# Optimization experiments

Hardware: AMD Instinct MI355X
Metric: run time of the kernel (lower is better)

Reference implementation:

```python
import jax, jax.numpy as jnp
import numpy as np
import math

KMAX = 4
K_FLOOR = 1e-6
NUM_GRAPHS = 32

def _k_lattice():
    r = np.arange(-KMAX, KMAX + 1)
    I, J, Kk = np.meshgrid(r, r, r, indexing='ij')
    lat = np.stack([I, J, Kk], axis=-1).reshape(-1, 3).astype(np.float32)
    lat = lat[np.any(lat != 0, axis=1)]  # exclude k=0 (include_k0=False)
    return jnp.asarray(lat)  # [K,3], K=728

def setup_inputs() -> dict:
    key = jax.random.key(0)
    ks = jax.random.split(key, 10)
    N, B, C, H = 8192, NUM_GRAPHS, 4, 64
    pos = jax.random.uniform(ks[0], (N, 3), dtype=jnp.float32) * 10.0
    batch = jnp.sort(jax.random.randint(ks[1], (N,), 0, B)).astype(jnp.int32)
    cell = jnp.eye(3, dtype=jnp.float32)[None] * 12.0 + 0.2 * jax.random.normal(ks[2], (B, 3, 3), dtype=jnp.float32)
    source = 0.1 * jax.random.normal(ks[3], (N, C), dtype=jnp.float32)
    W1 = jax.random.normal(ks[4], (3, H), dtype=jnp.float32) * (1.0 / math.sqrt(3))
    b1 = jnp.zeros((H,), jnp.float32)
    W2 = jax.random.normal(ks[5], (H, H), dtype=jnp.float32) * (1.0 / math.sqrt(H))
    b2 = jnp.zeros((H,), jnp.float32)
    W3 = jax.random.normal(ks[6], (H, 1), dtype=jnp.float32) * (1.0 / math.sqrt(H))
    b3 = jnp.zeros((1,), jnp.float32)
    return {"pos": pos, "batch": batch, "cell": cell, "source": source,
            "W1": W1, "b1": b1, "W2": W2, "b2": b2, "W3": W3, "b3": b3}

def reference(pos, batch, cell, source, W1, b1, W2, b2, W3, b3):
    two_pi = 2.0 * math.pi
    klat = _k_lattice()                              # [K,3]
    B = cell.shape[0]
    inv_cells = jnp.linalg.inv(cell)                 # [B,3,3]
    # fractional coords and phases
    frac = jnp.einsum('ni,nij->nj', pos, inv_cells[batch])   # [N,3]
    phases = two_pi * (frac @ klat.T)                # [N,K]
    cosP = jnp.cos(phases)
    sinP = jnp.sin(phases)
    # structure factors via segment-sum over graphs
    w_cos = source[:, None, :] * cosP[:, :, None]    # [N,K,C]
    w_sin = source[:, None, :] * sinP[:, :, None]
    S_cos = jax.ops.segment_sum(w_cos, batch, num_segments=B)  # [B,K,C]
    S_sin = jax.ops.segment_sum(w_sin, batch, num_segments=B)
    # k-space radial filter
    k_cart = two_pi * jnp.einsum('kd,bdh->bkh', klat, inv_cells)  # [B,K,3]
    k_norms = jnp.linalg.norm(k_cart, axis=-1)       # [B,K]
    safe_k = jnp.maximum(k_norms, K_FLOOR)
    x0 = jnp.log1p(safe_k)
    feat = jnp.stack([x0, x0 * x0, 1.0 / safe_k], axis=-1)       # [B,K,3]
    h = jax.nn.silu(feat @ W1 + b1)
    h = jax.nn.silu(h @ W2 + b2)
    scale = jax.nn.softplus((h @ W3 + b3)[..., 0])   # [B,K]
    w = (4.0 * math.pi / (safe_k * safe_k)) * scale
    w = jnp.where(k_norms > K_FLOOR, w, 0.0)         # include_k0=False
    volumes = jnp.maximum(jnp.abs(jnp.linalg.det(cell)), K_FLOOR)  # [B]
    # per-atom potential
    t_cos = w[batch] * cosP                          # [N,K]
    t_sin = w[batch] * sinP
    potential = (jnp.einsum('nk,nkc->nc', t_cos, S_cos[batch]) +
                 jnp.einsum('nk,nkc->nc', t_sin, S_sin[batch])) / volumes[batch][:, None]
    atom_energy = 0.5 * jnp.sum(source * potential, axis=-1, keepdims=True)  # [N,1]
    return atom_energy
```

## Files before the change

### kernel.cpp

```cpp
#include <hip/hip_runtime.h>
#include <math.h>

#define N_ATOMS 8192
#define NGRAPH  32
#define KHALF   364
#define TWO_PI  6.28318530717958647692f


__device__ __forceinline__ float silu_f(float x) {
    return x / (1.0f + __expf(-x));
}

__device__ __forceinline__ void screv(float rev, float* s, float* c) {
    float f = rev - floorf(rev);
    *s = __builtin_amdgcn_sinf(f);
    *c = __builtin_amdgcn_cosf(f);
}

__device__ __forceinline__ void inv3x3(const float* __restrict__ c, float* iv, float* detOut) {
    float a00 = c[0], a01 = c[1], a02 = c[2];
    float a10 = c[3], a11 = c[4], a12 = c[5];
    float a20 = c[6], a21 = c[7], a22 = c[8];
    float c00 = a11 * a22 - a12 * a21;
    float c01 = a12 * a20 - a10 * a22;
    float c02 = a10 * a21 - a11 * a20;
    float det = a00 * c00 + a01 * c01 + a02 * c02;
    float r = 1.0f / det;
    iv[0] = c00 * r; iv[1] = (a02 * a21 - a01 * a22) * r; iv[2] = (a01 * a12 - a02 * a11) * r;
    iv[3] = c01 * r; iv[4] = (a00 * a22 - a02 * a20) * r; iv[5] = (a02 * a10 - a00 * a12) * r;
    iv[6] = c02 * r; iv[7] = (a01 * a20 - a00 * a21) * r; iv[8] = (a00 * a11 - a01 * a10) * r;
    *detOut = det;
}

__device__ __forceinline__ int lower_bound_wave(const int* __restrict__ batch, int v, int lane) {
    int x = batch[lane * 128];
    int c1 = __popcll(__ballot(x < v));
    int lo2 = (c1 > 0 ? c1 - 1 : 0) * 128;
    int y = batch[lo2 + lane * 2];
    int c2 = __popcll(__ballot(y < v));
    if (c2 == 0) return lo2;
    int cand = lo2 + 2 * c2;
    return (batch[cand - 1] < v) ? cand : cand - 1;
}

__device__ __forceinline__ void tab_fill(float2* __restrict__ t9, float c1, float s1) {
    float c2 = c1 * c1 - s1 * s1, s2 = 2.f * c1 * s1;
    float c3 = c2 * c1 - s2 * s1, s3 = c2 * s1 + s2 * c1;
    float c4 = c2 * c2 - s2 * s2, s4 = 2.f * c2 * s2;
    t9[4] = make_float2(1.f, 0.f);
    t9[5] = make_float2(c1, s1);
    t9[3] = make_float2(c1, -s1);
    t9[6] = make_float2(c2, s2);
    t9[2] = make_float2(c2, -s2);
    t9[7] = make_float2(c3, s3);
    t9[1] = make_float2(c3, -s3);
    t9[8] = make_float2(c4, s4);
    t9[0] = make_float2(c4, -s4);
}

__global__ __launch_bounds__(512) void kAll(
    const float* __restrict__ cell, const float* __restrict__ pos,
    const int* __restrict__ batch, const float* __restrict__ source,
    const float* __restrict__ W1, const float* __restrict__ b1,
    const float* __restrict__ W2, const float* __restrict__ b2,
    const float* __restrict__ W3, const float* __restrict__ b3,
    float* __restrict__ out)
{
    __shared__ float2 tab[128][3][9];
    __shared__ float4 srcs[128];
    __shared__ float4 partC[7][64];
    __shared__ float4 partS[7][64];
    __shared__ float  comb[512];
    __shared__ int    sbounds[2];
    __shared__ float  lw[64];
    __shared__ float4 lSc[64];
    __shared__ float4 lSs[64];

    int bid = blockIdx.x;
    int tid = threadIdx.x;
    int gb = bid >> 3;
    int b  = bid & 7;

    int pA, jA0, jA1, jB0, jB1, nsegA, nel;
    if (b < 4) { pA = b;     jA0 = 0; jA1 = 5; jB0 = 0; jB1 = 0; nsegA = 45; nel = 45; }
    else       { pA = b - 4; jA0 = 5; jA1 = 9;
                 jB0 = b - 4; jB1 = (b == 7) ? 5 : (b - 3);
                 nsegA = 36; nel = 36 + (jB1 - jB0) * 9; }
    int nrows  = (jA1 - jA0) + (jB1 - jB0);
    int rsplit = (nrows + 1) >> 1;

    int kl = tid & 63;
    int h  = tid >> 6;

    if (h >= 6) {
        int lb = lower_bound_wave(batch, gb + (h - 6), kl);
        if (kl == 0) sbounds[h - 6] = lb;
    }

    float iv[9]; float det;
    inv3x3(cell + gb * 9, iv, &det);
    float vol = fmaxf(fabsf(det), 1e-6f);

    int el = kl;
    int pe, jje, lle;
    if (el < nsegA) { pe = pA; jje = jA0 + el / 9; lle = el % 9; }
    else            { int e2 = el - nsegA; pe = 4; jje = jB0 + e2 / 9; lle = e2 % 9; }
    int hk = pe * 81 + jje * 9 + lle;
    bool evalid = (el < nel) && (hk < KHALF);

    {
        float fi = (float)(pe - 4);
        float fj = (float)(jje - 4);
        float fl = (float)(lle - 4);
        float kx = TWO_PI * (fi * iv[0] + fj * iv[3] + fl * iv[6]);
        float ky = TWO_PI * (fi * iv[1] + fj * iv[4] + fl * iv[7]);
        float kz = TWO_PI * (fi * iv[2] + fj * iv[5] + fl * iv[8]);
        float kn = sqrtf(kx * kx + ky * ky + kz * kz);
        float sk = fmaxf(kn, 1e-6f);
        float x0 = log1pf(sk);
        float f0 = x0, f1 = x0 * x0, f2 = 1.0f / sk;

        float acc[8];
        #pragma unroll
        for (int j = 0; j < 8; ++j) acc[j] = b2[h * 8 + j];
        for (int i = 0; i < 64; ++i) {
            float a = b1[i] + f0 * W1[i] + f1 * W1[64 + i] + f2 * W1[128 + i];
            float hh = silu_f(a);
            const float* w2row = W2 + i * 64 + h * 8;
            #pragma unroll
            for (int j = 0; j < 8; ++j) acc[j] = fmaf(hh, w2row[j], acc[j]);
        }
        float partial = 0.f;
        #pragma unroll
        for (int j = 0; j < 8; ++j) partial += silu_f(acc[j]) * W3[h * 8 + j];
        comb[tid] = partial;
        __syncthreads();
        if (h == 0) {
            float mlp = b3[0];
            #pragma unroll
            for (int w = 0; w < 8; ++w) mlp += comb[kl + 64 * w];
            float sc = (mlp > 20.0f) ? mlp : log1pf(__expf(mlp));
            float wgt = (12.566370614359172954f / (sk * sk)) * sc;
            if (!(kn > 1e-6f)) wgt = 0.0f;
            lw[kl] = evalid ? (wgt / vol) : 0.0f;
        }
    }

    int s0 = sbounds[0], e0 = sbounds[1];

    float4 accC = make_float4(0.f, 0.f, 0.f, 0.f);
    float4 accS = make_float4(0.f, 0.f, 0.f, 0.f);

    for (int base = s0; base < e0; base += 128) {
        int cnt = min(128, e0 - base);
        __syncthreads();
        {
            int a    = tid & 127;
            int dsel = tid >> 7;
            if (a < cnt) {
                int n = base + a;
                if (dsel < 3) {
                    float px = pos[n * 3], py = pos[n * 3 + 1], pz = pos[n * 3 + 2];
                    float ph = px * iv[dsel] + py * iv[3 + dsel] + pz * iv[6 + dsel];
                    float s1, c1; screv(ph, &s1, &c1);
                    tab_fill(&tab[a][dsel][0], c1, s1);
                } else {
                    srcs[a] = ((const float4*)source)[n];
                }
            }
        }
        __syncthreads();

        if (evalid) {
            for (int a = h; a < cnt; a += 8) {
                float2 ti = tab[a][0][pe];
                float2 tj = tab[a][1][jje];
                float2 tl = tab[a][2][lle];
                float c12 = ti.x * tj.x - ti.y * tj.y;
                float s12 = ti.x * tj.y + ti.y * tj.x;
                float cv = c12 * tl.x - s12 * tl.y;
                float sv = c12 * tl.y + s12 * tl.x;
                float4 s = srcs[a];
                accC.x = fmaf(s.x, cv, accC.x); accC.y = fmaf(s.y, cv, accC.y);
                accC.z = fmaf(s.z, cv, accC.z); accC.w = fmaf(s.w, cv, accC.w);
                accS.x = fmaf(s.x, sv, accS.x); accS.y = fmaf(s.y, sv, accS.y);
                accS.z = fmaf(s.z, sv, accS.z); accS.w = fmaf(s.w, sv, accS.w);
            }
        }
    }

    if (h > 0) {
        partC[h - 1][kl] = accC;
        partS[h - 1][kl] = accS;
    }
    __syncthreads();
    if (h == 0) {
        #pragma unroll
        for (int qq = 0; qq < 7; ++qq) {
            float4 pc = partC[qq][kl], ps = partS[qq][kl];
            accC.x += pc.x; accC.y += pc.y; accC.z += pc.z; accC.w += pc.w;
            accS.x += ps.x; accS.y += ps.y; accS.z += ps.z; accS.w += ps.w;
        }
        lSc[kl] = accC;
        lSs[kl] = accS;
    }
    __syncthreads();

    int half = tid >> 8;
    int r0 = half ? rsplit : 0;
    int r1 = half ? nrows  : rsplit;
    int g = 4 - pA;

    for (int na = (tid & 255); s0 + na < e0; na += 256) {
        int n = s0 + na;
        float px = pos[n * 3], py = pos[n * 3 + 1], pz = pos[n * 3 + 2];
        float p1 = px * iv[0] + py * iv[3] + pz * iv[6];
        float p2 = px * iv[1] + py * iv[4] + pz * iv[7];
        float p3 = px * iv[2] + py * iv[5] + pz * iv[8];
        float s1, c1; screv(p1, &s1, &c1);
        float s2, c2; screv(p2, &s2, &c2);
        float s3, c3; screv(p3, &s3, &c3);
        float c3_2 = c3 * c3 - s3 * s3, s3_2 = 2.f * c3 * s3;
        float c3_4 = c3_2 * c3_2 - s3_2 * s3_2, s3_4 = 2.f * c3_2 * s3_2;
        float c2_2 = c2 * c2 - s2 * s2, s2_2 = 2.f * c2 * s2;
        float c2_4 = c2_2 * c2_2 - s2_2 * s2_2, s2_4 = 2.f * c2_2 * s2_2;
        float4 s = ((const float4*)source)[n];

        float acc = 0.f;
        int rr = 0;

        {
            float cg_, sg_;
            if (g == 1)      { cg_ = c1; sg_ = s1; }
            else {
                float c2p = c1 * c1 - s1 * s1, s2p = 2.f * c1 * s1;
                if (g == 2)      { cg_ = c2p; sg_ = s2p; }
                else if (g == 3) { cg_ = c2p * c1 - s2p * s1; sg_ = s2p * c1 + c2p * s1; }
                else             { cg_ = c2p * c2p - s2p * s2p; sg_ = 2.f * c2p * s2p; }
            }
            float ci0 = cg_, si0 = -sg_;

            float ejc, ejs;
            if (jA0 == 0) {
                ejc = ci0 * c2_4 + si0 * s2_4;
                ejs = si0 * c2_4 - ci0 * s2_4;
            } else {
                ejc = ci0 * c2 - si0 * s2;
                ejs = si0 * c2 + ci0 * s2;
            }

            for (int jj = jA0; jj < jA1; ++jj, ++rr) {
                if (rr >= r0 && rr < r1) {
                    float fc = ejc * c3_4 + ejs * s3_4;
                    float fs = ejs * c3_4 - ejc * s3_4;
                    #pragma unroll
                    for (int ll = 0; ll < 9; ++ll) {
                        int e = rr * 9 + ll;
                        float4 C  = lSc[e];
                        float4 S4 = lSs[e];
                        float w_ = lw[e];
                        float dc = s.x * C.x  + s.y * C.y  + s.z * C.z  + s.w * C.w;
                        float ds = s.x * S4.x + s.y * S4.y + s.z * S4.z + s.w * S4.w;
                        acc = fmaf(w_, fmaf(fc, dc, fs * ds), acc);
                        float nfc = fc * c3 - fs * s3;
                        fs = fc * s3 + fs * c3;
                        fc = nfc;
                    }
                }
                float nejc = ejc * c2 - ejs * s2;
                ejs = ejc * s2 + ejs * c2;
                ejc = nejc;
            }
        }

        if (jB1 > jB0) {
            float ejc = c2_4, ejs = -s2_4;
            for (int t = 0; t < jB0; ++t) {
                float nf = ejc * c2 - ejs * s2;
                ejs = ejc * s2 + ejs * c2;
                ejc = nf;
            }
            for (int jj = jB0; jj < jB1; ++jj, ++rr) {
                if (rr >= r0 && rr < r1) {
                    float fc = ejc * c3_4 + ejs * s3_4;
                    float fs = ejs * c3_4 - ejc * s3_4;
                    #pragma unroll
                    for (int ll = 0; ll < 9; ++ll) {
                        int e = rr * 9 + ll;
                        float4 C  = lSc[e];
                        float4 S4 = lSs[e];
                        float w_ = lw[e];
                        float dc = s.x * C.x  + s.y * C.y  + s.z * C.z  + s.w * C.w;
                        float ds = s.x * S4.x + s.y * S4.y + s.z * S4.z + s.w * S4.w;
                        acc = fmaf(w_, fmaf(fc, dc, fs * ds), acc);
                        float nfc = fc * c3 - fs * s3;
                        fs = fc * s3 + fs * c3;
                        fc = nfc;
                    }
                }
                float nejc = ejc * c2 - ejs * s2;
                ejs = ejc * s2 + ejs * c2;
                ejc = nejc;
            }
        }

        atomicAdd(&out[n], acc);
    }
}

extern "C" void kernel_launch(void* const* d_in, const int* in_sizes, int n_in,
                              void* d_out, int out_size, void* d_ws, size_t ws_size,
                              hipStream_t stream)
{
    const float* pos    = (const float*)d_in[0];
    const int*   batch  = (const int*)d_in[1];
    const float* cell   = (const float*)d_in[2];
    const float* source = (const float*)d_in[3];
    const float* W1 = (const float*)d_in[4];
    const float* b1 = (const float*)d_in[5];
    const float* W2 = (const float*)d_in[6];
    const float* b2 = (const float*)d_in[7];
    const float* W3 = (const float*)d_in[8];
    const float* b3 = (const float*)d_in[9];
    float* out = (float*)d_out;
    (void)d_ws; (void)ws_size;

    kAll<<<dim3(NGRAPH * 8), 512, 0, stream>>>(cell, pos, batch, source,
        W1, b1, W2, b2, W3, b3, out);
}
```

Before: 92.97 us.

## Stage per-atom phase tables once and reuse them in potential phase

Enlarges the atom chunk to 384 so a typical graph of about 256 atoms fits in one pass. Each atom's phase table is built once per block, holding only the rows this block needs, and is reused by both the structure-factor and potential phases instead of recomputing sin/cos per atom. MLP weights are copied into shared memory, global atom loads are issued before the MLP so their latency overlaps it, and the softplus reduction moves to wave 1. This adds a large shared-memory footprint with launch_bounds(512,1), keeps a fallback path for graphs over 384 atoms, and removes the block barrier inside the MLP.

```diff
diff --git a/kernel.cpp b/kernel.cpp
--- a/kernel.cpp
+++ b/kernel.cpp
@@ -5,6 +5,7 @@
 #define NGRAPH  32
 #define KHALF   364
 #define TWO_PI  6.28318530717958647692f
+#define CH      384
 
 
 __device__ __forceinline__ float silu_f(float x) {
@@ -43,22 +44,58 @@
     return (batch[cand - 1] < v) ? cand : cand - 1;
 }
 
-__device__ __forceinline__ void tab_fill(float2* __restrict__ t9, float c1, float s1) {
-    float c2 = c1 * c1 - s1 * s1, s2 = 2.f * c1 * s1;
-    float c3 = c2 * c1 - s2 * s1, s3 = c2 * s1 + s2 * c1;
-    float c4 = c2 * c2 - s2 * s2, s4 = 2.f * c2 * s2;
-    t9[4] = make_float2(1.f, 0.f);
-    t9[5] = make_float2(c1, s1);
-    t9[3] = make_float2(c1, -s1);
-    t9[6] = make_float2(c2, s2);
-    t9[2] = make_float2(c2, -s2);
-    t9[7] = make_float2(c3, s3);
-    t9[1] = make_float2(c3, -s3);
-    t9[8] = make_float2(c4, s4);
-    t9[0] = make_float2(c4, -s4);
-}
-
-__global__ __launch_bounds__(512) void kAll(
+__device__ __forceinline__ void stage_atom(
+    float2 (* __restrict__ atab)[17], float4* __restrict__ srcs, int a,
+    float px, float py, float pz, float4 msrc, const float* __restrict__ iv,
+    int g, int jA0, int jA1, int jB0, int jB1)
+{
+    float r1 = px * iv[0] + py * iv[3] + pz * iv[6];
+    float r2 = px * iv[1] + py * iv[4] + pz * iv[7];
+    float r3 = px * iv[2] + py * iv[5] + pz * iv[8];
+    float s1, c1; screv(r1, &s1, &c1);
+    float s2, c2; screv(r2, &s2, &c2);
+    float s3, c3; screv(r3, &s3, &c3);
+    float c1_2 = c1 * c1 - s1 * s1, s1_2 = 2.f * c1 * s1;
+    float cg_, sg_;
+    if (g == 1)      { cg_ = c1;   sg_ = s1; }
+    else if (g == 2) { cg_ = c1_2; sg_ = s1_2; }
+    else if (g == 3) { cg_ = c1_2 * c1 - s1_2 * s1; sg_ = s1_2 * c1 + c1_2 * s1; }
+    else             { cg_ = c1_2 * c1_2 - s1_2 * s1_2; sg_ = 2.f * c1_2 * s1_2; }
+    atab[a][0] = make_float2(cg_, -sg_);
+    float c2_2 = c2 * c2 - s2 * s2, s2_2 = 2.f * c2 * s2;
+    float c2_4 = c2_2 * c2_2 - s2_2 * s2_2, s2_4 = 2.f * c2_2 * s2_2;
+    float ec, es;
+    if (jA0 == 0) { ec = c2_4; es = -s2_4; } else { ec = c2; es = s2; }
+    int slot = 1;
+    for (int m = jA0; m < jA1; ++m) {
+        atab[a][slot] = make_float2(ec, es); ++slot;
+        float t = ec * c2 - es * s2; es = ec * s2 + es * c2; ec = t;
+    }
+    if (jB1 > jB0) {
+        int q = 4 - jB0;
+        float qc, qs;
+        if (q == 4)      { qc = c2_4; qs = s2_4; }
+        else if (q == 3) { qc = c2_2 * c2 - s2_2 * s2; qs = s2_2 * c2 + c2_2 * s2; }
+        else if (q == 2) { qc = c2_2; qs = s2_2; }
+        else             { qc = c2;   qs = s2; }
+        ec = qc; es = -qs;
+        for (int m = jB0; m < jB1; ++m) {
+            atab[a][slot] = make_float2(ec, es); ++slot;
+            float t = ec * c2 - es * s2; es = ec * s2 + es * c2; ec = t;
+        }
+    }
+    float c3_2 = c3 * c3 - s3 * s3, s3_2 = 2.f * c3 * s3;
+    float c3_4 = c3_2 * c3_2 - s3_2 * s3_2, s3_4 = 2.f * c3_2 * s3_2;
+    ec = c3_4; es = -s3_4;
+    #pragma unroll
+    for (int m = 0; m < 9; ++m) {
+        atab[a][7 + m] = make_float2(ec, es);
+        float t = ec * c3 - es * s3; es = ec * s3 + es * c3; ec = t;
+    }
+    srcs[a] = msrc;
+}
+
+__global__ __launch_bounds__(512, 1) void kAll(
     const float* __restrict__ cell, const float* __restrict__ pos,
     const int* __restrict__ batch, const float* __restrict__ source,
     const float* __restrict__ W1, const float* __restrict__ b1,
@@ -66,15 +103,16 @@
     const float* __restrict__ W3, const float* __restrict__ b3,
     float* __restrict__ out)
 {
-    __shared__ float2 tab[128][3][9];
-    __shared__ float4 srcs[128];
+    __shared__ float  lwts[4484];
+    __shared__ float2 atab[CH][17];
+    __shared__ float4 srcs[CH];
     __shared__ float4 partC[7][64];
     __shared__ float4 partS[7][64];
     __shared__ float  comb[512];
-    __shared__ int    sbounds[2];
     __shared__ float  lw[64];
     __shared__ float4 lSc[64];
     __shared__ float4 lSs[64];
+    __shared__ int    sbounds[2];
 
     int bid = blockIdx.x;
     int tid = threadIdx.x;
@@ -86,13 +124,25 @@
     else       { pA = b - 4; jA0 = 5; jA1 = 9;
                  jB0 = b - 4; jB1 = (b == 7) ? 5 : (b - 3);
                  nsegA = 36; nel = 36 + (jB1 - jB0) * 9; }
-    int nrows  = (jA1 - jA0) + (jB1 - jB0);
-    int rsplit = (nrows + 1) >> 1;
+    int nrA   = jA1 - jA0;
+    int nrows = nrA + (jB1 - jB0);
+    int g = 4 - pA;
 
     int kl = tid & 63;
     int h  = tid >> 6;
 
-    if (h >= 6) {
+    if (h < 6) {
+        for (int i = tid; i < 1120; i += 384) {
+            float4 v; int o;
+            if (i < 48)        { v = ((const float4*)W1)[i];      o = i * 4; }
+            else if (i < 64)   { v = ((const float4*)b1)[i - 48]; o = 192 + (i - 48) * 4; }
+            else if (i < 1088) { v = ((const float4*)W2)[i - 64]; o = 256 + (i - 64) * 4; }
+            else if (i < 1104) { v = ((const float4*)b2)[i - 1088]; o = 4352 + (i - 1088) * 4; }
+            else               { v = ((const float4*)W3)[i - 1104]; o = 4416 + (i - 1104) * 4; }
+            *((float4*)&lwts[o]) = v;
+        }
+        if (tid == 0) lwts[4480] = b3[0];
+    } else {
         int lb = lower_bound_wave(batch, gb + (h - 6), kl);
         if (kl == 0) sbounds[h - 6] = lb;
     }
@@ -105,9 +155,26 @@
     int pe, jje, lle;
     if (el < nsegA) { pe = pA; jje = jA0 + el / 9; lle = el % 9; }
     else            { int e2 = el - nsegA; pe = 4; jje = jB0 + e2 / 9; lle = e2 % 9; }
+    int rrl = el / 9;
     int hk = pe * 81 + jje * 9 + lle;
     bool evalid = (el < nel) && (hk < KHALF);
 
+    __syncthreads();
+
+    int s0 = sbounds[0], e0 = sbounds[1];
+    int len = e0 - s0;
+    int cnt0 = min(CH, len);
+    bool multi = len > CH;
+
+    float px0 = 0.f, py0 = 0.f, pz0 = 0.f;
+    float4 msrc = make_float4(0.f, 0.f, 0.f, 0.f);
+    if (tid < cnt0) {
+        int n = s0 + tid;
+        px0 = pos[n * 3]; py0 = pos[n * 3 + 1]; pz0 = pos[n * 3 + 2];
+        msrc = ((const float4*)source)[n];
+    }
+
+    float kn, sk;
     {
         float fi = (float)(pe - 4);
         float fj = (float)(jje - 4);
@@ -115,71 +182,75 @@
         float kx = TWO_PI * (fi * iv[0] + fj * iv[3] + fl * iv[6]);
         float ky = TWO_PI * (fi * iv[1] + fj * iv[4] + fl * iv[7]);
         float kz = TWO_PI * (fi * iv[2] + fj * iv[5] + fl * iv[8]);
-        float kn = sqrtf(kx * kx + ky * ky + kz * kz);
-        float sk = fmaxf(kn, 1e-6f);
+        kn = sqrtf(kx * kx + ky * ky + kz * kz);
+        sk = fmaxf(kn, 1e-6f);
         float x0 = log1pf(sk);
         float f0 = x0, f1 = x0 * x0, f2 = 1.0f / sk;
 
         float acc[8];
         #pragma unroll
-        for (int j = 0; j < 8; ++j) acc[j] = b2[h * 8 + j];
+        for (int j = 0; j < 8; ++j) acc[j] = lwts[4352 + h * 8 + j];
         for (int i = 0; i < 64; ++i) {
-            float a = b1[i] + f0 * W1[i] + f1 * W1[64 + i] + f2 * W1[128 + i];
-            float hh = silu_f(a);
-            const float* w2row = W2 + i * 64 + h * 8;
+            float a_ = lwts[192 + i] + f0 * lwts[i] + f1 * lwts[64 + i] + f2 * lwts[128 + i];
+            float hh = silu_f(a_);
+            const float* w2row = &lwts[256 + i * 64 + h * 8];
             #pragma unroll
             for (int j = 0; j < 8; ++j) acc[j] = fmaf(hh, w2row[j], acc[j]);
         }
         float partial = 0.f;
         #pragma unroll
-        for (int j = 0; j < 8; ++j) partial += silu_f(acc[j]) * W3[h * 8 + j];
+        for (int j = 0; j < 8; ++j) partial += silu_f(acc[j]) * lwts[4416 + h * 8 + j];
         comb[tid] = partial;
-        __syncthreads();
-        if (h == 0) {
-            float mlp = b3[0];
-            #pragma unroll
-            for (int w = 0; w < 8; ++w) mlp += comb[kl + 64 * w];
-            float sc = (mlp > 20.0f) ? mlp : log1pf(__expf(mlp));
-            float wgt = (12.566370614359172954f / (sk * sk)) * sc;
-            if (!(kn > 1e-6f)) wgt = 0.0f;
-            lw[kl] = evalid ? (wgt / vol) : 0.0f;
-        }
-    }
-
-    int s0 = sbounds[0], e0 = sbounds[1];
+    }
+
+    if (tid < cnt0)
+        stage_atom(atab, srcs, tid, px0, py0, pz0, msrc, iv, g, jA0, jA1, jB0, jB1);
+    __syncthreads();
 
     float4 accC = make_float4(0.f, 0.f, 0.f, 0.f);
     float4 accS = make_float4(0.f, 0.f, 0.f, 0.f);
-
-    for (int base = s0; base < e0; base += 128) {
-        int cnt = min(128, e0 - base);
+    if (evalid) {
+        for (int a = h; a < cnt0; a += 8) {
+            float2 tj = atab[a][1 + rrl];
+            float2 tl = atab[a][7 + lle];
+            float tic, tis;
+            if (el < nsegA) {
+                float2 fI = atab[a][0];
+                tic = fI.x * tj.x - fI.y * tj.y;
+                tis = fI.x * tj.y + fI.y * tj.x;
+            } else { tic = tj.x; tis = tj.y; }
+            float cv = tic * tl.x - tis * tl.y;
+            float sv = tic * tl.y + tis * tl.x;
+            float4 s = srcs[a];
+            accC.x = fmaf(s.x, cv, accC.x); accC.y = fmaf(s.y, cv, accC.y);
+            accC.z = fmaf(s.z, cv, accC.z); accC.w = fmaf(s.w, cv, accC.w);
+            accS.x = fmaf(s.x, sv, accS.x); accS.y = fmaf(s.y, sv, accS.y);
+            accS.z = fmaf(s.z, sv, accS.z); accS.w = fmaf(s.w, sv, accS.w);
+        }
+    }
+
+    for (int base = s0 + CH; base < e0; base += CH) {
+        int cnt = min(CH, e0 - base);
         __syncthreads();
-        {
-            int a    = tid & 127;
-            int dsel = tid >> 7;
-            if (a < cnt) {
-                int n = base + a;
-                if (dsel < 3) {
-                    float px = pos[n * 3], py = pos[n * 3 + 1], pz = pos[n * 3 + 2];
-                    float ph = px * iv[dsel] + py * iv[3 + dsel] + pz * iv[6 + dsel];
-                    float s1, c1; screv(ph, &s1, &c1);
-                    tab_fill(&tab[a][dsel][0], c1, s1);
-                } else {
-                    srcs[a] = ((const float4*)source)[n];
-                }
-            }
+        if (tid < cnt) {
+            int n = base + tid;
+            float px = pos[n * 3], py = pos[n * 3 + 1], pz = pos[n * 3 + 2];
+            float4 ms = ((const float4*)source)[n];
+            stage_atom(atab, srcs, tid, px, py, pz, ms, iv, g, jA0, jA1, jB0, jB1);
         }
         __syncthreads();
-
         if (evalid) {
             for (int a = h; a < cnt; a += 8) {
-                float2 ti = tab[a][0][pe];
-                float2 tj = tab[a][1][jje];
-                float2 tl = tab[a][2][lle];
-                float c12 = ti.x * tj.x - ti.y * tj.y;
-                float s12 = ti.x * tj.y + ti.y * tj.x;
-                float cv = c12 * tl.x - s12 * tl.y;
-                float sv = c12 * tl.y + s12 * tl.x;
+                float2 tj = atab[a][1 + rrl];
+                float2 tl = atab[a][7 + lle];
+                float tic, tis;
+                if (el < nsegA) {
+                    float2 fI = atab[a][0];
+                    tic = fI.x * tj.x - fI.y * tj.y;
+                    tis = fI.x * tj.y + fI.y * tj.x;
+                } else { tic = tj.x; tis = tj.y; }
+                float cv = tic * tl.x - tis * tl.y;
+                float sv = tic * tl.y + tis * tl.x;
                 float4 s = srcs[a];
                 accC.x = fmaf(s.x, cv, accC.x); accC.y = fmaf(s.y, cv, accC.y);
                 accC.z = fmaf(s.z, cv, accC.z); accC.w = fmaf(s.w, cv, accC.w);
@@ -203,108 +274,129 @@
         }
         lSc[kl] = accC;
         lSs[kl] = accS;
+    } else if (h == 1) {
+        float mlp = lwts[4480];
+        #pragma unroll
+        for (int w = 0; w < 8; ++w) mlp += comb[kl + 64 * w];
+        float sc = (mlp > 20.0f) ? mlp : log1pf(__expf(mlp));
+        float wgt = (12.566370614359172954f / (sk * sk)) * sc;
+        if (!(kn > 1e-6f)) wgt = 0.0f;
+        lw[kl] = evalid ? (wgt / vol) : 0.0f;
     }
     __syncthreads();
 
     int half = tid >> 8;
+    int rsplit = (nrows + 1) >> 1;
     int r0 = half ? rsplit : 0;
     int r1 = half ? nrows  : rsplit;
-    int g = 4 - pA;
-
-    for (int na = (tid & 255); s0 + na < e0; na += 256) {
-        int n = s0 + na;
-        float px = pos[n * 3], py = pos[n * 3 + 1], pz = pos[n * 3 + 2];
-        float p1 = px * iv[0] + py * iv[3] + pz * iv[6];
-        float p2 = px * iv[1] + py * iv[4] + pz * iv[7];
-        float p3 = px * iv[2] + py * iv[5] + pz * iv[8];
-        float s1, c1; screv(p1, &s1, &c1);
-        float s2, c2; screv(p2, &s2, &c2);
-        float s3, c3; screv(p3, &s3, &c3);
-        float c3_2 = c3 * c3 - s3 * s3, s3_2 = 2.f * c3 * s3;
-        float c3_4 = c3_2 * c3_2 - s3_2 * s3_2, s3_4 = 2.f * c3_2 * s3_2;
-        float c2_2 = c2 * c2 - s2 * s2, s2_2 = 2.f * c2 * s2;
-        float c2_4 = c2_2 * c2_2 - s2_2 * s2_2, s2_4 = 2.f * c2_2 * s2_2;
-        float4 s = ((const float4*)source)[n];
-
-        float acc = 0.f;
-        int rr = 0;
-
-        {
-            float cg_, sg_;
-            if (g == 1)      { cg_ = c1; sg_ = s1; }
-            else {
-                float c2p = c1 * c1 - s1 * s1, s2p = 2.f * c1 * s1;
-                if (g == 2)      { cg_ = c2p; sg_ = s2p; }
-                else if (g == 3) { cg_ = c2p * c1 - s2p * s1; sg_ = s2p * c1 + c2p * s1; }
-                else             { cg_ = c2p * c2p - s2p * s2p; sg_ = 2.f * c2p * s2p; }
+
+    if (!multi) {
+        for (int na = (tid & 255); na < len; na += 256) {
+            float2 fI = atab[na][0];
+            float4 s  = srcs[na];
+            float acc = 0.f;
+            for (int rr = r0; rr < r1; ++rr) {
+                float2 tj = atab[na][1 + rr];
+                float rjc, rjs;
+                if (rr < nrA) {
+                    rjc = fI.x * tj.x - fI.y * tj.y;
+                    rjs = fI.x * tj.y + fI.y * tj.x;
+                } else {
+                    rjc = tj.x; rjs = tj.y;
+                }
+                #pragma unroll
+                for (int ll = 0; ll < 9; ++ll) {
+                    float2 tl = atab[na][7 + ll];
+                    float fc = rjc * tl.x - rjs * tl.y;
+                    float fs = rjc * tl.y + rjs * tl.x;
+                    int e = rr * 9 + ll;
+                    float4 C  = lSc[e];
+                    float4 S4 = lSs[e];
+                    float w_  = lw[e];
+                    float dc = s.x * C.x  + s.y * C.y  + s.z * C.z  + s.w * C.w;
+                    float ds = s.x * S4.x + s.y * S4.y + s.z * S4.z + s.w * S4.w;
+                    acc = fmaf(w_, fmaf(fc, dc, fs * ds), acc);
+                }
             }
-            float ci0 = cg_, si0 = -sg_;
-
-            float ejc, ejs;
-            if (jA0 == 0) {
-                ejc = ci0 * c2_4 + si0 * s2_4;
-                ejs = si0 * c2_4 - ci0 * s2_4;
-            } else {
-                ejc = ci0 * c2 - si0 * s2;
-                ejs = si0 * c2 + ci0 * s2;
+            atomicAdd(&out[s0 + na], acc);
+        }
+    } else {
+        for (int na = (tid & 255); na < len; na += 256) {
+            int n = s0 + na;
+            float px = pos[n * 3], py = pos[n * 3 + 1], pz = pos[n * 3 + 2];
+            float r1v = px * iv[0] + py * iv[3] + pz * iv[6];
+            float r2v = px * iv[1] + py * iv[4] + pz * iv[7];
+            float r3v = px * iv[2] + py * iv[5] + pz * iv[8];
+            float s1, c1; screv(r1v, &s1, &c1);
+            float s2, c2; screv(r2v, &s2, &c2);
+            float s3, c3; screv(r3v, &s3, &c3);
+            float c3_2 = c3 * c3 - s3 * s3, s3_2 = 2.f * c3 * s3;
+            float c3_4 = c3_2 * c3_2 - s3_2 * s3_2, s3_4 = 2.f * c3_2 * s3_2;
+            float c2_2 = c2 * c2 - s2 * s2, s2_2 = 2.f * c2 * s2;
+            float c2_4 = c2_2 * c2_2 - s2_2 * s2_2, s2_4 = 2.f * c2_2 * s2_2;
+            float4 s = ((const float4*)source)[n];
+            float acc = 0.f;
+            int rr = 0;
+            {
+                float c1_2 = c1 * c1 - s1 * s1, s1_2 = 2.f * c1 * s1;
+                float cg_, sg_;
+                if (g == 1)      { cg_ = c1;   sg_ = s1; }
+                else if (g == 2) { cg_ = c1_2; sg_ = s1_2; }
+                else if (g == 3) { cg_ = c1_2 * c1 - s1_2 * s1; sg_ = s1_2 * c1 + c1_2 * s1; }
+                else             { cg_ = c1_2 * c1_2 - s1_2 * s1_2; sg_ = 2.f * c1_2 * s1_2; }
+                float ci0 = cg_, si0 = -sg_;
+                float ejc, ejs;
+                if (jA0 == 0) { ejc = ci0 * c2_4 + si0 * s2_4; ejs = si0 * c2_4 - ci0 * s2_4; }
+                else          { ejc = ci0 * c2 - si0 * s2;     ejs = si0 * c2 + ci0 * s2; }
+                for (int jj = jA0; jj < jA1; ++jj, ++rr) {
+                    if (rr >= r0 && rr < r1) {
+                        float fc = ejc * c3_4 + ejs * s3_4;
+                        float fs = ejs * c3_4 - ejc * s3_4;
+                        #pragma unroll
+                        for (int ll = 0; ll < 9; ++ll) {
+                            int e = rr * 9 + ll;
+                            float4 C  = lSc[e];
+                            float4 S4 = lSs[e];
+                            float w_  = lw[e];
+                            float dc = s.x * C.x  + s.y * C.y  + s.z * C.z  + s.w * C.w;
+                            float ds = s.x * S4.x + s.y * S4.y + s.z * S4.z + s.w * S4.w;
+                            acc = fmaf(w_, fmaf(fc, dc, fs * ds), acc);
+                            float nfc = fc * c3 - fs * s3;
+                            fs = fc * s3 + fs * c3;
+                            fc = nfc;
+                        }
+                    }
+                    float t = ejc * c2 - ejs * s2; ejs = ejc * s2 + ejs * c2; ejc = t;
+                }
             }
-
-            for (int jj = jA0; jj < jA1; ++jj, ++rr) {
-                if (rr >= r0 && rr < r1) {
-                    float fc = ejc * c3_4 + ejs * s3_4;
-                    float fs = ejs * c3_4 - ejc * s3_4;
-                    #pragma unroll
-                    for (int ll = 0; ll < 9; ++ll) {
-                        int e = rr * 9 + ll;
-                        float4 C  = lSc[e];
-                        float4 S4 = lSs[e];
-                        float w_ = lw[e];
-                        float dc = s.x * C.x  + s.y * C.y  + s.z * C.z  + s.w * C.w;
-                        float ds = s.x * S4.x + s.y * S4.y + s.z * S4.z + s.w * S4.w;
-                        acc = fmaf(w_, fmaf(fc, dc, fs * ds), acc);
-                        float nfc = fc * c3 - fs * s3;
-                        fs = fc * s3 + fs * c3;
-                        fc = nfc;
+            if (jB1 > jB0) {
+                float ejc = c2_4, ejs = -s2_4;
+                for (int t2 = 0; t2 < jB0; ++t2) {
+                    float t = ejc * c2 - ejs * s2; ejs = ejc * s2 + ejs * c2; ejc = t;
+                }
+                for (int jj = jB0; jj < jB1; ++jj, ++rr) {
+                    if (rr >= r0 && rr < r1) {
+                        float fc = ejc * c3_4 + ejs * s3_4;
+                        float fs = ejs * c3_4 - ejc * s3_4;
+                        #pragma unroll
+                        for (int ll = 0; ll < 9; ++ll) {
+                            int e = rr * 9 + ll;
+                            float4 C  = lSc[e];
+                            float4 S4 = lSs[e];
+                            float w_  = lw[e];
+                            float dc = s.x * C.x  + s.y * C.y  + s.z * C.z  + s.w * C.w;
+                            float ds = s.x * S4.x + s.y * S4.y + s.z * S4.z + s.w * S4.w;
+                            acc = fmaf(w_, fmaf(fc, dc, fs * ds), acc);
+                            float nfc = fc * c3 - fs * s3;
+                            fs = fc * s3 + fs * c3;
+                            fc = nfc;
+                        }
                     }
+                    float t = ejc * c2 - ejs * s2; ejs = ejc * s2 + ejs * c2; ejc = t;
                 }
-                float nejc = ejc * c2 - ejs * s2;
-                ejs = ejc * s2 + ejs * c2;
-                ejc = nejc;
             }
-        }
-
-        if (jB1 > jB0) {
-            float ejc = c2_4, ejs = -s2_4;
-            for (int t = 0; t < jB0; ++t) {
-                float nf = ejc * c2 - ejs * s2;
-                ejs = ejc * s2 + ejs * c2;
-                ejc = nf;
-            }
-            for (int jj = jB0; jj < jB1; ++jj, ++rr) {
-                if (rr >= r0 && rr < r1) {
-                    float fc = ejc * c3_4 + ejs * s3_4;
-                    float fs = ejs * c3_4 - ejc * s3_4;
-                    #pragma unroll
-                    for (int ll = 0; ll < 9; ++ll) {
-                        int e = rr * 9 + ll;
-                        float4 C  = lSc[e];
-                        float4 S4 = lSs[e];
-                        float w_ = lw[e];
-                        float dc = s.x * C.x  + s.y * C.y  + s.z * C.z  + s.w * C.w;
-                        float ds = s.x * S4.x + s.y * S4.y + s.z * S4.z + s.w * S4.w;
-                        acc = fmaf(w_, fmaf(fc, dc, fs * ds), acc);
-                        float nfc = fc * c3 - fs * s3;
-                        fs = fc * s3 + fs * c3;
-                        fc = nfc;
-                    }
-                }
-                float nejc = ejc * c2 - ejs * s2;
-                ejs = ejc * s2 + ejs * c2;
-                ejc = nejc;
-            }
-        }
-
-        atomicAdd(&out[n], acc);
+            atomicAdd(&out[n], acc);
+        }
     }
 }
 
```

After: 91.46 us. Within noise of the previous version (-1.6%).
